# Performance work log

Hardware: AMD Instinct MI355X
Metric: run time of the kernel (lower is better)

## Reference

```python
import jax, jax.numpy as jnp
import numpy as np

DIM = 1024
HEADS = 16
DIM_HEAD = 64
INNER = HEADS * DIM_HEAD
LN_EPS = 1e-5


def setup_inputs() -> dict:
    key = jax.random.key(0)
    ks = jax.random.split(key, 7)
    b, n = 2, 2048
    x = jax.random.normal(ks[0], (b, n, DIM), dtype=jnp.float32)
    attn_bias = jax.random.normal(ks[1], (HEADS, n, n), dtype=jnp.float32)
    gamma = jnp.ones((DIM,), dtype=jnp.float32)
    beta = jnp.zeros((DIM,), dtype=jnp.float32)
    wq = jax.random.normal(ks[2], (DIM, INNER), dtype=jnp.float32) * (DIM ** -0.5)
    wkv = jax.random.normal(ks[3], (DIM, 2 * INNER), dtype=jnp.float32) * (DIM ** -0.5)
    wo = jax.random.normal(ks[4], (INNER, DIM), dtype=jnp.float32) * (INNER ** -0.5)
    return {"x": x, "attn_bias": attn_bias, "gamma": gamma, "beta": beta,
            "wq": wq, "wkv": wkv, "wo": wo}


def reference(x, attn_bias, gamma, beta, wq, wkv, wo):
    b, n, _ = x.shape
    scale = DIM_HEAD ** -0.5
    # LayerNorm
    mu = jnp.mean(x, axis=-1, keepdims=True)
    var = jnp.var(x, axis=-1, keepdims=True)
    xn = (x - mu) * jax.lax.rsqrt(var + LN_EPS) * gamma + beta
    # QKV projections
    q = xn @ wq                      # [b, n, inner]
    kv = xn @ wkv                    # [b, n, 2*inner]
    k, v = jnp.split(kv, 2, axis=-1)
    split_heads = lambda t: t.reshape(b, n, HEADS, DIM_HEAD).transpose(0, 2, 1, 3)
    q, k, v = map(split_heads, (q, k, v))  # [b, h, n, d]
    q = q * scale
    sim = jnp.einsum('bhid,bhjd->bhij', q, k)
    sim = sim + attn_bias[None]      # broadcast over batch
    causal_mask = jnp.triu(jnp.ones((n, n), dtype=bool), k=1)
    sim = jnp.where(causal_mask, -jnp.finfo(sim.dtype).max, sim)
    attn = jax.nn.softmax(sim, axis=-1)
    out = jnp.einsum('bhij,bhjd->bhid', attn, v)
    out = out.transpose(0, 2, 1, 3).reshape(b, n, INNER)
    return out @ wo
```

## Files before the change

### kernel.cpp

```cpp
#include <hip/hip_runtime.h>
#include <hip/hip_bf16.h>

#define DIM   1024
#define HEADS 16
#define DHEAD 64
#define INNER 1024
#define NSEQ  2048
#define NB    2
#define MROWS (NB * NSEQ)
#define QS    (3 * INNER)

typedef __attribute__((ext_vector_type(8))) short    short8;
typedef __attribute__((ext_vector_type(4))) short    short4v;
typedef __attribute__((ext_vector_type(4))) float    floatx4;
typedef __attribute__((ext_vector_type(8))) _Float16 half8;

#define GLOBAL_AS __attribute__((address_space(1)))
#define LDS_AS    __attribute__((address_space(3)))

static __device__ __forceinline__ short f2h(float f) {
  _Float16 h = (_Float16)f;
  return __builtin_bit_cast(short, h);
}
static __device__ __forceinline__ float h2f(short s) {
  return (float)__builtin_bit_cast(_Float16, s);
}

static __device__ __forceinline__ floatx4 mfma16(short8 a, short8 b, floatx4 c) {
  return __builtin_amdgcn_mfma_f32_16x16x32_f16(
      __builtin_bit_cast(half8, a), __builtin_bit_cast(half8, b), c, 0, 0, 0);
}

static __device__ __forceinline__ int xcd_work(int bid, int nwg) {
  int q = nwg >> 3, r = nwg & 7;
  int xcd = bid & 7, pos = bid >> 3;
  return (xcd < r ? xcd * (q + 1) : r * (q + 1) + (xcd - r) * q) + pos;
}

__device__ __constant__ signed char kQtTab[40] = {
  15,14,13,12,11,10,9,8,7,6,5,4,3,
  15,14,13,12,11,10,9,8,7,
  15,14,13,12,11,
  15,
  2,6,10,14,
  1,5,9,13,
  0,4,8,12};
__device__ __constant__ signed char kCTab[40] = {
  0,0,0,0,0,0,0,0,0,0,0,0,0,
  1,1,1,1,1,1,1,1,1,
  2,2,2,2,2,
  3,
  0,1,2,3,
  0,1,2,3,
  0,1,2,3};
__device__ __constant__ signed char kSlotTab[16][4] = {
  {36,-1,-1,-1},{32,-1,-1,-1},{28,-1,-1,-1},{12,-1,-1,-1},
  {11,37,-1,-1},{10,33,-1,-1},{ 9,29,-1,-1},{ 8,21,-1,-1},
  { 7,20,38,-1},{ 6,19,34,-1},{ 5,18,30,-1},{ 4,17,26,-1},
  { 3,16,25,39},{ 2,15,24,35},{ 1,14,23,31},{ 0,13,22,27}};

__global__ __launch_bounds__(256) void prep_kernel(
    const float* __restrict__ x, const float* __restrict__ gamma,
    const float* __restrict__ beta, short* __restrict__ xn,
    const float* __restrict__ wq, const float* __restrict__ wkv,
    const float* __restrict__ wo, short* __restrict__ wqkv_t,
    short* __restrict__ wo_t) {
  __shared__ float tile[32][33];
  int bid = blockIdx.x;
  int t = threadIdx.x;

  if (bid < MROWS) {
    const float4* xr = reinterpret_cast<const float4*>(x + (size_t)bid * DIM);
    float4 v = xr[t];
    float s  = v.x + v.y + v.z + v.w;
    float s2 = v.x * v.x + v.y * v.y + v.z * v.z + v.w * v.w;
#pragma unroll
    for (int off = 1; off < 64; off <<= 1) {
      s  += __shfl_xor(s, off);
      s2 += __shfl_xor(s2, off);
    }
    float* red = &tile[0][0];
    if ((t & 63) == 0) { red[t >> 6] = s; red[(t >> 6) + 4] = s2; }
    __syncthreads();
    s  = red[0] + red[1] + red[2] + red[3];
    s2 = red[4] + red[5] + red[6] + red[7];
    float mu   = s * (1.0f / DIM);
    float var  = s2 * (1.0f / DIM) - mu * mu;
    float rstd = rsqrtf(var + 1e-5f);
    float4 g  = reinterpret_cast<const float4*>(gamma)[t];
    float4 bb = reinterpret_cast<const float4*>(beta)[t];
    short4v o;
    o.x = f2h((v.x - mu) * rstd * g.x + bb.x);
    o.y = f2h((v.y - mu) * rstd * g.y + bb.y);
    o.z = f2h((v.z - mu) * rstd * g.z + bb.z);
    o.w = f2h((v.w - mu) * rstd * g.w + bb.w);
    reinterpret_cast<short4v*>(xn + (size_t)bid * DIM)[t] = o;
    return;
  }

  bid -= MROWS;
  const float* src; short* dst; int Nn, nx;
  if (bid < 1024)      { src = wq;  dst = wqkv_t;                     Nn = 1024; nx = 32; }
  else if (bid < 3072) { bid -= 1024; src = wkv;
                         dst = wqkv_t + (size_t)1024 * 1024;          Nn = 2048; nx = 64; }
  else                 { bid -= 3072; src = wo;  dst = wo_t;          Nn = 1024; nx = 32; }
  int n0 = (bid % nx) * 32, k0 = (bid / nx) * 32;
  int tx = t & 31, ty = t >> 5;
#pragma unroll
  for (int i = 0; i < 32; i += 8)
    tile[ty + i][tx] = src[(size_t)(k0 + ty + i) * Nn + n0 + tx];
  __syncthreads();
#pragma unroll
  for (int i = 0; i < 32; i += 8)
    dst[(size_t)(n0 + ty + i) * 1024 + k0 + tx] = f2h(tile[tx][ty + i]);
}

template <bool F32OUT>
__global__ __launch_bounds__(256) void gemm_cv(const short* __restrict__ A,
                                               const short* __restrict__ Bt,
                                               void* __restrict__ Cout,
                                               int Nn, int Kk, int NBN,
                                               float oscale, float oscale2,
                                               int qsplit) {
  __shared__ __attribute__((aligned(16))) short As[2][128 * 64];
  __shared__ __attribute__((aligned(16))) short Bs[2][128 * 64];
  int wk = xcd_work(blockIdx.x, gridDim.x);
  int bm = wk / NBN, bn = wk % NBN;
  int t = threadIdx.x, lane = t & 63, w = t >> 6;
  int l15 = lane & 15, lhi = lane >> 4;
  int wr = w >> 1, wc = w & 1;
  const short* Ag = A + (size_t)bm * 128 * Kk;
  const short* Bg = Bt + (size_t)bn * 128 * Kk;

  auto stage = [&](int kt, int buf) {
#pragma unroll
    for (int it = 0; it < 4; ++it) {
      int id = it * 256 + t;
      int row = id >> 3;
      int cs = ((id & 7) ^ (row & 7)) << 3;
      __builtin_amdgcn_global_load_lds(
          (const GLOBAL_AS unsigned int*)(Ag + (size_t)row * Kk + kt * 64 + cs),
          (LDS_AS unsigned int*)(&As[buf][id * 8]), 16, 0, 0);
    }
#pragma unroll
    for (int it = 0; it < 4; ++it) {
      int id = it * 256 + t;
      int row = id >> 3;
      int cs = ((id & 7) ^ (row & 7)) << 3;
      __builtin_amdgcn_global_load_lds(
          (const GLOBAL_AS unsigned int*)(Bg + (size_t)row * Kk + kt * 64 + cs),
          (LDS_AS unsigned int*)(&Bs[buf][id * 8]), 16, 0, 0);
    }
  };

  floatx4 acc[4][4] = {};
  int NK = Kk >> 6;

  stage(0, 0);
  stage(1, 1);
  for (int kt = 0; kt < NK; ++kt) {
    if (kt + 1 < NK) asm volatile("s_waitcnt vmcnt(8)" ::: "memory");
    else             asm volatile("s_waitcnt vmcnt(0)" ::: "memory");
    __builtin_amdgcn_s_barrier();
    __builtin_amdgcn_sched_barrier(0);

    int buf = kt & 1;
#pragma unroll
    for (int kc = 0; kc < 2; ++kc) {
      short8 a[4], b[4];
#pragma unroll
      for (int mt = 0; mt < 4; ++mt) {
        int row = wr * 64 + mt * 16 + l15;
        int g = (kc * 4 + lhi) ^ (l15 & 7);
        a[mt] = *reinterpret_cast<const short8*>(&As[buf][row * 64 + g * 8]);
      }
#pragma unroll
      for (int nt = 0; nt < 4; ++nt) {
        int row = wc * 64 + nt * 16 + l15;
        int g = (kc * 4 + lhi) ^ (l15 & 7);
        b[nt] = *reinterpret_cast<const short8*>(&Bs[buf][row * 64 + g * 8]);
      }
#pragma unroll
      for (int mt = 0; mt < 4; ++mt)
#pragma unroll
        for (int nt = 0; nt < 4; ++nt)
          acc[mt][nt] = mfma16(a[mt], b[nt], acc[mt][nt]);
    }

    asm volatile("s_waitcnt lgkmcnt(0)" ::: "memory");
    __builtin_amdgcn_sched_barrier(0);
    __builtin_amdgcn_s_barrier();
    __builtin_amdgcn_sched_barrier(0);
    if (kt + 2 < NK) stage(kt + 2, buf);
  }

  int row0 = bm * 128 + wr * 64;
  int col0 = bn * 128 + wc * 64;
#pragma unroll
  for (int mt = 0; mt < 4; ++mt)
#pragma unroll
    for (int nt = 0; nt < 4; ++nt) {
      float osc = (col0 + nt * 16 < qsplit) ? oscale : oscale2;
#pragma unroll
      for (int r = 0; r < 4; ++r) {
        int row = row0 + mt * 16 + lhi * 4 + r;
        int col = col0 + nt * 16 + l15;
        if (F32OUT)
          ((float*)Cout)[(size_t)row * Nn + col] = acc[mt][nt][r] * osc;
        else
          ((short*)Cout)[(size_t)row * Nn + col] = f2h(acc[mt][nt][r] * osc);
      }
    }
}

__global__ __launch_bounds__(512) void attn_kernel(const short* __restrict__ qkv,
                                                   const float* __restrict__ bias,
                                                   short* __restrict__ ao,
                                                   short* __restrict__ Opart,
                                                   float* __restrict__ mlpart) {
  __shared__ __attribute__((aligned(16))) short Ks[2][2][4096];
  __shared__ __attribute__((aligned(16))) short Vt[2][4096];
  __shared__ __attribute__((aligned(16))) short Ps[128 * 72];

  int p = blockIdx.x;
  int rank = p >> 4, h = p & 15;
  int qt = kQtTab[rank], c = kCTab[rank];
  int tt0 = c * 8;
  int tt1 = 2 * qt + 2; if (tt0 + 8 < tt1) tt1 = tt0 + 8;
  int qb = qt * 128;
  int t = threadIdx.x, lane = t & 63, w = t >> 6;
  int l15 = lane & 15, lhi = lane >> 4;

  short8 qf[2][2];
#pragma unroll
  for (int bb = 0; bb < 2; ++bb) {
    const short* qrow = qkv +
        ((size_t)(bb * NSEQ + qb + w * 16 + l15)) * QS + h * DHEAD + lhi * 8;
    qf[bb][0] = *reinterpret_cast<const short8*>(qrow);
    qf[bb][1] = *reinterpret_cast<const short8*>(qrow + 32);
  }

  int krow = t >> 3;
  int kcg  = (t & 7) ^ (krow & 7);
  int vrr = (t >> 4) * 2, vcc = (t & 15) << 2;
  short4v vr[2][2];

  auto issueK = [&](int tile, int nb) {
#pragma unroll
    for (int bb = 0; bb < 2; ++bb) {
      const short* gp = qkv +
          ((size_t)(bb * NSEQ + tile * 64 + krow)) * QS + INNER + h * DHEAD + kcg * 8;
      __builtin_amdgcn_global_load_lds(
          (const GLOBAL_AS unsigned int*)gp,
          (LDS_AS unsigned int*)(&Ks[nb][bb][0] + (size_t)w * 512), 16, 0, 0);
    }
  };
  auto issueV = [&](int tile) {
#pragma unroll
    for (int bb = 0; bb < 2; ++bb) {
      const short* vp = qkv + ((size_t)(bb * NSEQ + tile * 64 + vrr)) * QS +
                        2 * INNER + h * DHEAD + vcc;
      vr[bb][0] = *reinterpret_cast<const short4v*>(vp);
      vr[bb][1] = *reinterpret_cast<const short4v*>(vp + QS);
    }
  };
  auto writeV = [&]() {
#pragma unroll
    for (int bb = 0; bb < 2; ++bb)
#pragma unroll
      for (int e = 0; e < 4; ++e) {
        int d  = vcc + e;
        int jj = vrr ^ ((d & 7) << 3);
        unsigned int pk = (unsigned short)vr[bb][0][e] |
                          ((unsigned int)(unsigned short)vr[bb][1][e] << 16);
        *reinterpret_cast<unsigned int*>(&Vt[bb][d * 64 + jj]) = pk;
      }
  };
  auto issueB = [&](int tile, floatx4 (&br)[4]) {
    const float* bb0 = bias +
        ((size_t)h * NSEQ + (qb + w * 16 + l15)) * NSEQ + tile * 64 + lhi * 4;
#pragma unroll
    for (int jt = 0; jt < 4; ++jt)
      br[jt] = *reinterpret_cast<const floatx4*>(bb0 + jt * 16);
  };

  float m[2], l[2];
  floatx4 oacc[2][4] = {};
#pragma unroll
  for (int bb = 0; bb < 2; ++bb) { m[bb] = -1e30f; l[bb] = 0.f; }

  int swz = (l15 & 7) << 3;

  auto step = [&](int tt, int KB, floatx4 (&brU)[4], floatx4 (&brN)[4]) {
    bool more = (tt + 1 < tt1);
    if (more) { issueK(tt + 1, KB ^ 1); issueV(tt + 1); issueB(tt + 1, brN); }

#pragma unroll
    for (int bb = 0; bb < 2; ++bb) {
      floatx4 s[4];
#pragma unroll
      for (int jt = 0; jt < 4; ++jt) s[jt] = brU[jt];

#pragma unroll
      for (int jt = 0; jt < 4; ++jt) {
        int ro = (jt * 16 + l15) * 64;
        short8 k0 = *reinterpret_cast<const short8*>(
            &Ks[KB][bb][ro + ((lhi * 8) ^ swz)]);
        short8 k1 = *reinterpret_cast<const short8*>(
            &Ks[KB][bb][ro + ((lhi * 8 + 32) ^ swz)]);
        s[jt] = mfma16(k0, qf[bb][0], s[jt]);
        s[jt] = mfma16(k1, qf[bb][1], s[jt]);
      }

      if (tt >= 2 * qt) {
        int dq = qb + w * 16 + l15 - tt * 64;
#pragma unroll
        for (int jt = 0; jt < 4; ++jt)
#pragma unroll
          for (int r = 0; r < 4; ++r)
            if (jt * 16 + lhi * 4 + r > dq) s[jt][r] = -1e30f;
      }

      float mx = s[0][0];
#pragma unroll
      for (int jt = 0; jt < 4; ++jt)
#pragma unroll
        for (int r = 0; r < 4; ++r) mx = fmaxf(mx, s[jt][r]);
      mx = fmaxf(mx, __shfl_xor(mx, 16));
      mx = fmaxf(mx, __shfl_xor(mx, 32));
      float mnew = fmaxf(m[bb], mx);
      float fac  = __expf(m[bb] - mnew);
      m[bb] = mnew;
      float ps = 0.f;
#pragma unroll
      for (int jt = 0; jt < 4; ++jt)
#pragma unroll
        for (int r = 0; r < 4; ++r) {
          float pv = __expf(s[jt][r] - mnew);
          s[jt][r] = pv;
          ps += pv;
        }
      ps += __shfl_xor(ps, 16);
      ps += __shfl_xor(ps, 32);
      l[bb] = l[bb] * fac + ps;

      float facr[4];
#pragma unroll
      for (int r = 0; r < 4; ++r)
        facr[r] = __shfl(fac, (lane & 48) | (lhi * 4 + r));
#pragma unroll
      for (int dt = 0; dt < 4; ++dt)
#pragma unroll
        for (int r = 0; r < 4; ++r) oacc[bb][dt][r] *= facr[r];

#pragma unroll
      for (int jt = 0; jt < 4; ++jt) {
        short4v pv4;
        pv4.x = f2h(s[jt][0]); pv4.y = f2h(s[jt][1]);
        pv4.z = f2h(s[jt][2]); pv4.w = f2h(s[jt][3]);
        *reinterpret_cast<short4v*>(
            &Ps[(w * 16 + l15) * 72 + jt * 16 + lhi * 4]) = pv4;
      }

#pragma unroll
      for (int jc = 0; jc < 2; ++jc) {
        short8 pf = *reinterpret_cast<const short8*>(
            &Ps[(w * 16 + l15) * 72 + lhi * 8 + jc * 32]);
#pragma unroll
        for (int dt = 0; dt < 4; ++dt) {
          int dd = dt * 16 + l15;
          short8 vf = *reinterpret_cast<const short8*>(
              &Vt[bb][dd * 64 + ((lhi * 8 + jc * 32) ^ swz)]);
          oacc[bb][dt] = mfma16(pf, vf, oacc[bb][dt]);
        }
      }
    }

    if (more) {
      __syncthreads();
      writeV();
      __syncthreads();
    }
  };

  floatx4 brA[4], brB[4];
  issueK(tt0, 0);
  issueV(tt0);
  issueB(tt0, brA);
  __syncthreads();
  writeV();
  __syncthreads();

  int nt = tt1 - tt0;
  for (int i = 0; i < nt; i += 2) {
    step(tt0 + i, 0, brA, brB);
    step(tt0 + i + 1, 1, brB, brA);
  }

  bool single = (tt0 == 0) && (tt1 == 2 * qt + 2);
  if (single) {
#pragma unroll
    for (int bb = 0; bb < 2; ++bb) {
      float linv = 1.f / l[bb];
      float lr[4];
#pragma unroll
      for (int r = 0; r < 4; ++r)
        lr[r] = __shfl(linv, (lane & 48) | (lhi * 4 + r));
#pragma unroll
      for (int dt = 0; dt < 4; ++dt)
#pragma unroll
        for (int r = 0; r < 4; ++r) {
          int row = qb + w * 16 + lhi * 4 + r;
          int col = h * DHEAD + dt * 16 + l15;
          ao[((size_t)(bb * NSEQ + row)) * INNER + col] =
              f2h(oacc[bb][dt][r] * lr[r]);
        }
    }
  } else {
#pragma unroll
    for (int bb = 0; bb < 2; ++bb) {
      size_t pp = ((size_t)h * 40 + rank) * 2 + bb;
      short* Ob = Opart + pp * 8192;
#pragma unroll
      for (int dt = 0; dt < 4; ++dt)
#pragma unroll
        for (int r = 0; r < 4; ++r)
          Ob[(w * 16 + lhi * 4 + r) * 64 + dt * 16 + l15] = f2h(oacc[bb][dt][r]);
      if (lhi == 0) {
        mlpart[pp * 256 + w * 16 + l15] = m[bb];
        mlpart[pp * 256 + 128 + w * 16 + l15] = l[bb];
      }
    }
  }
}

__global__ __launch_bounds__(512) void attn_combine(const short* __restrict__ Opart,
                                                    const float* __restrict__ mlpart,
                                                    short* __restrict__ o) {
  int qt = blockIdx.x + 4, h = blockIdx.y, b = blockIdx.z;
  int nc = (2 * qt + 9) >> 3;
  int t = threadIdx.x, row = t >> 2, cg = (t & 3) << 4;

  float mv[4], lv[4];
  float M = -1e30f;
#pragma unroll
  for (int c2 = 0; c2 < 4; ++c2) {
    if (c2 < nc) {
      size_t pp = ((size_t)h * 40 + kSlotTab[qt][c2]) * 2 + b;
      mv[c2] = mlpart[pp * 256 + row];
      lv[c2] = mlpart[pp * 256 + 128 + row];
      M = fmaxf(M, mv[c2]);
    }
  }

  float acc[16] = {};
  float lsum = 0.f;
#pragma unroll
  for (int c2 = 0; c2 < 4; ++c2) {
    if (c2 >= nc) break;
    float wgt = __expf(mv[c2] - M);
    lsum += wgt * lv[c2];
    size_t pp = ((size_t)h * 40 + kSlotTab[qt][c2]) * 2 + b;
    const short8* Or =
        reinterpret_cast<const short8*>(Opart + pp * 8192 + row * 64 + cg);
    short8 a0 = Or[0], a1 = Or[1];
#pragma unroll
    for (int e = 0; e < 8; ++e) {
      acc[e]     += wgt * h2f(a0[e]);
      acc[8 + e] += wgt * h2f(a1[e]);
    }
  }
  float inv = 1.f / lsum;
  short* op = o + ((size_t)(b * NSEQ + qt * 128 + row)) * INNER + h * DHEAD + cg;
  short8 o0, o1;
#pragma unroll
  for (int e = 0; e < 8; ++e) {
    o0[e] = f2h(acc[e] * inv);
    o1[e] = f2h(acc[8 + e] * inv);
  }
  reinterpret_cast<short8*>(op)[0] = o0;
  reinterpret_cast<short8*>(op)[1] = o1;
}

extern "C" void kernel_launch(void* const* d_in, const int* in_sizes, int n_in,
                              void* d_out, int out_size, void* d_ws, size_t ws_size,
                              hipStream_t stream) {
  const float* x     = (const float*)d_in[0];
  const float* bias  = (const float*)d_in[1];
  const float* gamma = (const float*)d_in[2];
  const float* beta  = (const float*)d_in[3];
  const float* wq    = (const float*)d_in[4];
  const float* wkv   = (const float*)d_in[5];
  const float* wo    = (const float*)d_in[6];
  float* out = (float*)d_out;

  char* ws = (char*)d_ws;
  const size_t MB = 1024 * 1024;
  short* xn      = (short*)(ws);
  short* wqkv_t  = (short*)(ws + 8  * MB);
  short* wo_t    = (short*)(ws + 14 * MB);
  short* qkv     = (short*)(ws + 16 * MB);
  short* Opart   = (short*)(ws + 40 * MB);
  float* mlpart  = (float*)(ws + 62 * MB);
  short* ao      = xn;

  prep_kernel<<<8192, 256, 0, stream>>>(x, gamma, beta, xn, wq, wkv, wo,
                                        wqkv_t, wo_t);

  gemm_cv<false><<<(MROWS / 128) * (QS / 128), 256, 0, stream>>>(
      xn, wqkv_t, qkv, QS, DIM, QS / 128, 0.125f, 1.0f, 1024);

  attn_kernel<<<640, 512, 0, stream>>>(qkv, bias, ao, Opart, mlpart);
  attn_combine<<<dim3(12, HEADS, NB), 512, 0, stream>>>(Opart, mlpart, ao);

  gemm_cv<true><<<(MROWS / 128) * (DIM / 128), 256, 0, stream>>>(
      ao, wo_t, out, DIM, INNER, DIM / 128, 1.0f, 1.0f, 0);
}
```

Measured before the change: 151.8 us.

## Prefetch V two tiles ahead with double-buffered registers and fine-grained waitcnts

```diff
diff --git a/kernel.cpp b/kernel.cpp
--- a/kernel.cpp
+++ b/kernel.cpp
@@ -243,7 +243,6 @@
   int krow = t >> 3;
   int kcg  = (t & 7) ^ (krow & 7);
   int vrr = (t >> 4) * 2, vcc = (t & 15) << 2;
-  short4v vr[2][2];
 
   auto issueK = [&](int tile, int nb) {
 #pragma unroll
@@ -255,24 +254,24 @@
           (LDS_AS unsigned int*)(&Ks[nb][bb][0] + (size_t)w * 512), 16, 0, 0);
     }
   };
-  auto issueV = [&](int tile) {
+  auto issueV = [&](int tile, short4v (&dst)[2][2]) {
 #pragma unroll
     for (int bb = 0; bb < 2; ++bb) {
       const short* vp = qkv + ((size_t)(bb * NSEQ + tile * 64 + vrr)) * QS +
                         2 * INNER + h * DHEAD + vcc;
-      vr[bb][0] = *reinterpret_cast<const short4v*>(vp);
-      vr[bb][1] = *reinterpret_cast<const short4v*>(vp + QS);
+      dst[bb][0] = *reinterpret_cast<const short4v*>(vp);
+      dst[bb][1] = *reinterpret_cast<const short4v*>(vp + QS);
     }
   };
-  auto writeV = [&]() {
+  auto writeV = [&](short4v (&src)[2][2]) {
 #pragma unroll
     for (int bb = 0; bb < 2; ++bb)
 #pragma unroll
       for (int e = 0; e < 4; ++e) {
         int d  = vcc + e;
         int jj = vrr ^ ((d & 7) << 3);
-        unsigned int pk = (unsigned short)vr[bb][0][e] |
-                          ((unsigned int)(unsigned short)vr[bb][1][e] << 16);
+        unsigned int pk = (unsigned short)src[bb][0][e] |
+                          ((unsigned int)(unsigned short)src[bb][1][e] << 16);
         *reinterpret_cast<unsigned int*>(&Vt[bb][d * 64 + jj]) = pk;
       }
   };
@@ -290,10 +289,15 @@
   for (int bb = 0; bb < 2; ++bb) { m[bb] = -1e30f; l[bb] = 0.f; }
 
   int swz = (l15 & 7) << 3;
-
-  auto step = [&](int tt, int KB, floatx4 (&brU)[4], floatx4 (&brN)[4]) {
-    bool more = (tt + 1 < tt1);
-    if (more) { issueK(tt + 1, KB ^ 1); issueV(tt + 1); issueB(tt + 1, brN); }
+  int tlast = tt1 - 1;
+
+  auto step = [&](int tt, int KB, floatx4 (&brU)[4], floatx4 (&brN)[4],
+                  short4v (&vrI)[2][2], short4v (&vrW)[2][2]) {
+    int tK = (tt + 1 < tlast) ? tt + 1 : tlast;
+    int tV = (tt + 2 < tlast) ? tt + 2 : tlast;
+    issueK(tK, KB ^ 1);
+    issueV(tV, vrI);
+    issueB(tK, brN);
 
 #pragma unroll
     for (int bb = 0; bb < 2; ++bb) {
@@ -301,6 +305,7 @@
 #pragma unroll
       for (int jt = 0; jt < 4; ++jt) s[jt] = brU[jt];
 
+      __builtin_amdgcn_s_setprio(1);
 #pragma unroll
       for (int jt = 0; jt < 4; ++jt) {
         int ro = (jt * 16 + l15) * 64;
@@ -311,6 +316,7 @@
         s[jt] = mfma16(k0, qf[bb][0], s[jt]);
         s[jt] = mfma16(k1, qf[bb][1], s[jt]);
       }
+      __builtin_amdgcn_s_setprio(0);
 
       if (tt >= 2 * qt) {
         int dq = qb + w * 16 + l15 - tt * 64;
@@ -362,6 +368,7 @@
             &Ps[(w * 16 + l15) * 72 + jt * 16 + lhi * 4]) = pv4;
       }
 
+      __builtin_amdgcn_s_setprio(1);
 #pragma unroll
       for (int jc = 0; jc < 2; ++jc) {
         short8 pf = *reinterpret_cast<const short8*>(
@@ -374,27 +381,39 @@
           oacc[bb][dt] = mfma16(pf, vf, oacc[bb][dt]);
         }
       }
-    }
-
-    if (more) {
-      __syncthreads();
-      writeV();
-      __syncthreads();
-    }
+      __builtin_amdgcn_s_setprio(0);
+    }
+
+    asm volatile("s_waitcnt lgkmcnt(0)" ::: "memory");
+    __builtin_amdgcn_sched_barrier(0);
+    __builtin_amdgcn_s_barrier();
+    writeV(vrW);
+    asm volatile("s_waitcnt vmcnt(8) lgkmcnt(0)" ::: "memory");
+    __builtin_amdgcn_sched_barrier(0);
+    __builtin_amdgcn_s_barrier();
+    __builtin_amdgcn_sched_barrier(0);
   };
 
   floatx4 brA[4], brB[4];
+  short4v vrA[2][2], vrB[2][2];
+
+  issueV(tt0, vrA);
   issueK(tt0, 0);
-  issueV(tt0);
   issueB(tt0, brA);
-  __syncthreads();
-  writeV();
-  __syncthreads();
+  writeV(vrA);
+  {
+    int tV1 = (tt0 + 1 < tlast) ? tt0 + 1 : tlast;
+    issueV(tV1, vrB);
+  }
+  asm volatile("s_waitcnt vmcnt(8) lgkmcnt(0)" ::: "memory");
+  __builtin_amdgcn_sched_barrier(0);
+  __builtin_amdgcn_s_barrier();
+  __builtin_amdgcn_sched_barrier(0);
 
   int nt = tt1 - tt0;
   for (int i = 0; i < nt; i += 2) {
-    step(tt0 + i, 0, brA, brB);
-    step(tt0 + i + 1, 1, brB, brA);
+    step(tt0 + i,     0, brA, brB, vrA, vrB);
+    step(tt0 + i + 1, 1, brB, brA, vrB, vrA);
   }
 
   bool single = (tt0 == 0) && (tt1 == 2 * qt + 2);
```

Result: slower. 157.3 us (+3.7%).
